# Optimization experiments

Hardware: AMD Instinct MI355X
Metric: run time of the kernel (lower is better)

## Reference

```python
import jax, jax.numpy as jnp
import numpy as np

ENC = 50       # enc_units
TEMP = 5.0     # attention_temp
T = 20         # rollout steps
B = 262144


def setup_inputs() -> dict:
    key = jax.random.key(0)
    ks = jax.random.split(key, 16)
    u = lambda k, shape, lo, hi: jax.random.uniform(k, shape, minval=lo, maxval=hi, dtype=jnp.float32)
    n = lambda k, shape, s: jax.random.normal(k, shape, dtype=jnp.float32) * s
    return {
        "unscaled_s": u(ks[0], (B, T, 7), 0.1, 2.0),          # vel/dv/dx features, kept positive
        "z": n(ks[1], (B, 2), 1.0),
        "desired_v": u(ks[2], (B, 1), 10.0, 30.0),
        "desired_tgap": u(ks[3], (B, 1), 0.5, 2.0),
        "min_jamx": u(ks[4], (B, 1), 1.0, 4.0),
        "max_act": u(ks[5], (B, 1), 0.5, 3.0),
        "min_act": u(ks[6], (B, 1), 0.5, 3.0),
        "h0": n(ks[7], (B, ENC), 0.1),
        "c0": n(ks[8], (B, ENC), 0.1),
        "W_lstm": n(ks[9], (2, 4 * ENC), 0.3),
        "U_lstm": n(ks[10], (ENC, 4 * ENC), 0.1),
        "b_lstm": jnp.zeros((4 * ENC,), jnp.float32),
        "W_att": n(ks[11], (ENC, ENC), 0.1),
        "b_att": jnp.zeros((ENC,), jnp.float32),
        "W_neu": n(ks[12], (ENC, 1), 0.1),
        "b_neu": jnp.zeros((1,), jnp.float32),
    }


def reference(unscaled_s, z, desired_v, desired_tgap, min_jamx, max_act, min_act,
              h0, c0, W_lstm, U_lstm, b_lstm, W_att, b_att, W_neu, b_neu):
    def idm(vel, dv, dx):  # all [B,1]
        gap = min_jamx + desired_tgap * vel + vel * dv / (2.0 * jnp.sqrt(max_act * min_act))
        act = max_act * (1.0 - (vel / desired_v) ** 4 - (gap / dx) ** 2)
        return jnp.clip(act, -3.5, 3.5)

    # LSTM input z is the same every step: precompute input contribution once.
    xz = z @ W_lstm + b_lstm  # [B, 4*ENC]

    def step(carry, s_t):  # s_t: [B, 7]
        h, c = carry
        gates = xz + h @ U_lstm
        i, f, g, o = jnp.split(gates, 4, axis=-1)  # keras gate order i,f,c,o
        c = jax.nn.sigmoid(f) * c + jax.nn.sigmoid(i) * jnp.tanh(g)
        h = jax.nn.sigmoid(o) * jnp.tanh(c)
        att = jax.nn.sigmoid(TEMP * ((h @ W_att + b_att) @ W_neu + b_neu))  # [B,1]
        vel = s_t[:, 0:1]
        fl = idm(vel, s_t[:, 2:3], s_t[:, 3:4])
        fm = idm(vel, s_t[:, 5:6], s_t[:, 6:7])
        act = att * fl + (1.0 - att) * fm
        return (h, c), (act, att)

    (_, _), (acts, atts) = jax.lax.scan(step, (h0, c0), jnp.transpose(unscaled_s, (1, 0, 2)))
    act_seq = jnp.transpose(acts, (1, 0, 2))    # [B, T, 1]
    att_scores = jnp.transpose(atts, (1, 0, 2))  # [B, T, 1]
    return act_seq, att_scores
```

## Files before the change

### kernel.cpp

```cpp
#include <hip/hip_runtime.h>

#define ENC 50
#define NT 20
#define TEMPC 5.0f
#define HSTRIDE 72
#define L2E 1.4426950408889634f
#define NFRAG 26

typedef __attribute__((ext_vector_type(8))) short bf16x8;
typedef __attribute__((ext_vector_type(4))) float f32x4;

__device__ __forceinline__ unsigned short f2bf(float x) {
  union { float f; unsigned u; } cv; cv.f = x;
  unsigned u = cv.u;
  u += 0x7FFFu + ((u >> 16) & 1u);
  return (unsigned short)(u >> 16);
}

__global__ void idm_prep(const float* __restrict__ U, const float* __restrict__ Wl,
                         const float* __restrict__ bl, const float* __restrict__ Wa,
                         const float* __restrict__ ba, const float* __restrict__ Wn,
                         const float* __restrict__ bn,
                         unsigned short* __restrict__ Afrag, float* __restrict__ wcomb) {
  int tid = blockIdx.x * blockDim.x + threadIdx.x;
  for (int idx = tid; idx < NFRAG * 64; idx += blockDim.x * gridDim.x) {
    int frag = idx >> 6, lane = idx & 63;
    int m = frag >> 1, kt = frag & 1;
    int sub = lane & 15;
    int kbase = 32 * kt + 8 * (lane >> 4);
    int p = sub >> 2, q = sub & 3;
    int f = 4 * m + p;
    float sc = (q == 2) ? (2.0f * L2E) : (-L2E);
    unsigned short o[8];
#pragma unroll
    for (int e = 0; e < 8; ++e) {
      int k = kbase + e;
      float val = 0.f;
      if (f < ENC) {
        int col = q * ENC + f;
        if (k < ENC)            val = U[k * 4 * ENC + col];
        else if (k == ENC)      val = Wl[col];
        else if (k == ENC + 1)  val = Wl[4 * ENC + col];
        else if (k == ENC + 2)  val = bl[col];
      }
      o[e] = f2bf(val * sc);
    }
#pragma unroll
    for (int e = 0; e < 8; ++e) Afrag[idx * 8 + e] = o[e];
  }
  if (tid < 52) {
    float s = 0.f;
    if (tid < ENC) { for (int j = 0; j < ENC; ++j) s += Wa[tid * ENC + j] * Wn[j]; }
    wcomb[tid] = s * (-TEMPC * L2E);
  }
  if (tid == 52) {
    float s = bn[0];
    for (int j = 0; j < ENC; ++j) s += ba[j] * Wn[j];
    wcomb[52] = s * (-TEMPC * L2E);
  }
}

template <int PRE>
__global__ __launch_bounds__(256, 2) void idm_main(
    const float* __restrict__ s_in, const float* __restrict__ zin,
    const float* __restrict__ dvp, const float* __restrict__ tgp,
    const float* __restrict__ jxp, const float* __restrict__ map,
    const float* __restrict__ mip, const float* __restrict__ h0,
    const float* __restrict__ c0,
    const unsigned short* __restrict__ Afrag, const float* __restrict__ wcomb,
    const float* __restrict__ U, const float* __restrict__ Wl, const float* __restrict__ bl,
    const float* __restrict__ Wa, const float* __restrict__ ba,
    const float* __restrict__ Wn, const float* __restrict__ bn,
    float* __restrict__ out_act, float* __restrict__ out_att, int Btot) {
  __shared__ __align__(16) unsigned short hlds[4 * 16 * HSTRIDE];
  __shared__ float wcl[64];
  const int tid = threadIdx.x;
  const int wid = tid >> 6, lane = tid & 63;
  const int v = lane & 15, p = lane >> 4;
  int b = blockIdx.x * 64 + wid * 16 + v;
  if (b >= Btot) b = Btot - 1;

  bf16x8 A[13][2];
  float wc[13], bcomb;
  if (PRE) {
#pragma unroll
    for (int m = 0; m < 13; ++m) {
      A[m][0] = ((const bf16x8*)Afrag)[(2 * m) * 64 + lane];
      A[m][1] = ((const bf16x8*)Afrag)[(2 * m + 1) * 64 + lane];
    }
#pragma unroll
    for (int m = 0; m < 13; ++m) { int f = 4 * m + p; wc[m] = (f < ENC) ? wcomb[f] : 0.f; }
    bcomb = wcomb[52];
  } else {
    if (tid < 53) {
      float s;
      if (tid < ENC) {
        s = 0.f;
        for (int j = 0; j < ENC; ++j) s += Wa[tid * ENC + j] * Wn[j];
      } else if (tid < 52) {
        s = 0.f;
      } else {
        s = bn[0];
        for (int j = 0; j < ENC; ++j) s += ba[j] * Wn[j];
      }
      wcl[tid] = s * (-TEMPC * L2E);
    } else if (tid < 64) {
      wcl[tid] = 0.f;
    }
    __syncthreads();
#pragma unroll
    for (int m = 0; m < 13; ++m) {
#pragma unroll
      for (int kt = 0; kt < 2; ++kt) {
        const int pp = v >> 2, q = v & 3;
        const int fb = 4 * m + pp;
        const int kbase = 32 * kt + 8 * p;
        float sc = (q == 2) ? (2.0f * L2E) : (-L2E);
        bf16x8 a;
#pragma unroll
        for (int e = 0; e < 8; ++e) {
          int k = kbase + e;
          float val = 0.f;
          if (fb < ENC) {
            int col = q * ENC + fb;
            if (k < ENC)            val = U[k * 4 * ENC + col];
            else if (k == ENC)      val = Wl[col];
            else if (k == ENC + 1)  val = Wl[4 * ENC + col];
            else if (k == ENC + 2)  val = bl[col];
          }
          a[e] = (short)f2bf(val * sc);
        }
        A[m][kt] = a;
      }
    }
#pragma unroll
    for (int m = 0; m < 13; ++m) { int f = 4 * m + p; wc[m] = (f < ENC) ? wcl[f] : 0.f; }
    bcomb = wcl[52];
  }

  const float amax = map[b], amin = mip[b];
  const float tgap = tgp[b], jamx = jxp[b];
  const float inv_dv = __builtin_amdgcn_rcpf(dvp[b]);
  const float inv2s = 0.5f * __builtin_amdgcn_rsqf(amax * amin);

  float c[13];
#pragma unroll
  for (int m = 0; m < 13; ++m) {
    int f = 4 * m + p;
    c[m] = (f < ENC) ? c0[(size_t)b * ENC + f] : 0.f;
  }

  unsigned short* hl = &hlds[wid * 16 * HSTRIDE];
  for (int i = lane; i < 16 * HSTRIDE / 2; i += 64) ((unsigned*)hl)[i] = 0u;
#pragma unroll
  for (int m = 0; m < 13; ++m) {
    int f = 4 * m + p;
    if (f < ENC) hl[v * HSTRIDE + f] = f2bf(h0[(size_t)b * ENC + f]);
  }
  if (p == 0) {
    hl[v * HSTRIDE + 50] = f2bf(zin[(size_t)b * 2 + 0]);
    hl[v * HSTRIDE + 51] = f2bf(zin[(size_t)b * 2 + 1]);
    hl[v * HSTRIDE + 52] = (unsigned short)0x3F80;
  }

  const float* srow = s_in + (size_t)b * (NT * 7);
  const size_t ob = (size_t)b * NT;
  const bf16x8* hv = (const bf16x8*)hl;
  const int sel = 3 * (p & 1);

#pragma unroll 1
  for (int t = 0; t < NT; ++t) {
    bf16x8 B0 = hv[v * 9 + p];
    bf16x8 B1 = hv[v * 9 + 4 + p];
    f32x4 accbuf[2];
    {
      f32x4 z4 = {0.f, 0.f, 0.f, 0.f};
      f32x4 t0 = __builtin_amdgcn_mfma_f32_16x16x32_bf16(A[0][0], B0, z4, 0, 0, 0);
      accbuf[0] = __builtin_amdgcn_mfma_f32_16x16x32_bf16(A[0][1], B1, t0, 0, 0, 0);
    }
    float att_dot = 0.f;
#pragma unroll
    for (int m = 0; m < 13; ++m) {
      if (m < 12) {
        f32x4 z4 = {0.f, 0.f, 0.f, 0.f};
        f32x4 t0 = __builtin_amdgcn_mfma_f32_16x16x32_bf16(A[m + 1][0], B0, z4, 0, 0, 0);
        accbuf[(m + 1) & 1] = __builtin_amdgcn_mfma_f32_16x16x32_bf16(A[m + 1][1], B1, t0, 0, 0, 0);
      }
      f32x4 acc = accbuf[m & 1];
      float a  = __builtin_amdgcn_exp2f(acc[0]);
      float bb = __builtin_amdgcn_exp2f(acc[1]);
      float G  = __builtin_amdgcn_exp2f(acc[2]);
      float d  = __builtin_amdgcn_exp2f(acc[3]);
      float R = 1.f + a, P = 1.f + bb, Q = G + 1.f;
      float QR = Q * R;
      float num = fmaf(G - 1.f, P, c[m] * QR);
      float cn = num * __builtin_amdgcn_rcpf(P * QR);
      c[m] = cn;
      float C2 = __builtin_amdgcn_exp2f(cn * (2.0f * L2E));
      float hn = (C2 - 1.f) * __builtin_amdgcn_rcpf((C2 + 1.f) * (1.f + d));
      att_dot = fmaf(hn, wc[m], att_dot);
      int f = 4 * m + p;
      if (f < ENC) hl[v * HSTRIDE + f] = f2bf(hn);
    }
    att_dot += __shfl_xor(att_dot, 16, 64);
    att_dot += __shfl_xor(att_dot, 32, 64);
    float e2 = __builtin_amdgcn_exp2f(att_dot + bcomb);
    float att = __builtin_amdgcn_rcpf(1.f + e2);

    const float* sp = srow + t * 7;
    float vel = sp[0];
    float dvs = sp[2 + sel], dxs = sp[3 + sel];
    float r = vel * inv_dv;
    float r2 = r * r;
    float r4 = r2 * r2;
    float base = jamx + tgap * vel;
    float g = (base + vel * dvs * inv2s) * __builtin_amdgcn_rcpf(dxs);
    float fs = amax * (1.f - r4 - g * g);
    fs = fminf(fmaxf(fs, -3.5f), 3.5f);
    float fo = __shfl_xor(fs, 16, 64);
    float act = att * fs + (1.f - att) * fo;
    if (p == 0) {
      out_act[ob + t] = act;
      out_att[ob + t] = att;
    }
  }
}

extern "C" void kernel_launch(void* const* d_in, const int* in_sizes, int n_in,
                              void* d_out, int out_size, void* d_ws, size_t ws_size,
                              hipStream_t stream) {
  const float* s   = (const float*)d_in[0];
  const float* z   = (const float*)d_in[1];
  const float* dv  = (const float*)d_in[2];
  const float* tg  = (const float*)d_in[3];
  const float* jx  = (const float*)d_in[4];
  const float* ma  = (const float*)d_in[5];
  const float* mi  = (const float*)d_in[6];
  const float* h0  = (const float*)d_in[7];
  const float* c0  = (const float*)d_in[8];
  const float* Wl  = (const float*)d_in[9];
  const float* Ul  = (const float*)d_in[10];
  const float* bl  = (const float*)d_in[11];
  const float* Wa  = (const float*)d_in[12];
  const float* ba  = (const float*)d_in[13];
  const float* Wn  = (const float*)d_in[14];
  const float* bn  = (const float*)d_in[15];
  const int B = in_sizes[2];
  float* out_act = (float*)d_out;
  float* out_att = out_act + (size_t)B * NT;
  const int grid = (B + 63) / 64;
  const size_t need = (size_t)NFRAG * 64 * 8 * sizeof(unsigned short) + 64 * sizeof(float);
  if (d_ws && ws_size >= need) {
    unsigned short* Af = (unsigned short*)d_ws;
    float* wcb = (float*)(Af + NFRAG * 64 * 8);
    idm_prep<<<1, 256, 0, stream>>>(Ul, Wl, bl, Wa, ba, Wn, bn, Af, wcb);
    idm_main<1><<<grid, 256, 0, stream>>>(s, z, dv, tg, jx, ma, mi, h0, c0, Af, wcb,
                                          Ul, Wl, bl, Wa, ba, Wn, bn, out_act, out_att, B);
  } else {
    idm_main<0><<<grid, 256, 0, stream>>>(s, z, dv, tg, jx, ma, mi, h0, c0, nullptr, nullptr,
                                          Ul, Wl, bl, Wa, ba, Wn, bn, out_act, out_att, B);
  }
}
```

Measured before the change: 353.7 us.

## Move half of LSTM weight fragments to LDS and remap features for packed stores

Only 6 of the 13 weight-tile fragment pairs stay in registers; the other 7 are staged into shared memory once per block and read every step. This frees VGPRs so launch bounds can rise from 2 to 3 blocks per SM for more latency hiding. The hidden-feature layout is remapped to contiguous 13-feature chunks per lane group so pairs of h values can be stored as one packed bf16 word. In exchange, each step issues extra LDS reads on the serial recurrence path.

```diff
diff --git a/kernel.cpp b/kernel.cpp
--- a/kernel.cpp
+++ b/kernel.cpp
@@ -5,7 +5,9 @@
 #define TEMPC 5.0f
 #define HSTRIDE 72
 #define L2E 1.4426950408889634f
-#define NFRAG 26
+#define NTILE 13
+#define NREG 6
+#define NLDS 7
 
 typedef __attribute__((ext_vector_type(8))) short bf16x8;
 typedef __attribute__((ext_vector_type(4))) float f32x4;
@@ -15,6 +17,27 @@
   unsigned u = cv.u;
   u += 0x7FFFu + ((u >> 16) & 1u);
   return (unsigned short)(u >> 16);
+}
+
+__device__ __forceinline__ float a_elem(int m, int lane, int kt, int e,
+                                        const float* U, const float* Wl,
+                                        const float* bl) {
+  int sub = lane & 15;
+  int pa = sub >> 2, r = sub & 3;
+  int feat = 13 * pa + m;
+  int k = 32 * kt + 8 * (lane >> 4) + e;
+  float val = 0.f;
+  if (feat < ENC) {
+    int col = r * ENC + feat;
+    if (k < 56) {
+      int pk = k / 14, j = k - 14 * pk;
+      int fin = 13 * pk + j;
+      if (j < 13 && fin < ENC) val = U[fin * 4 * ENC + col];
+    } else if (k == 56) val = Wl[col];
+    else if (k == 57)   val = Wl[4 * ENC + col];
+    else if (k == 58)   val = bl[col];
+  }
+  return val * ((r == 2) ? (2.0f * L2E) : (-L2E));
 }
 
 __global__ void idm_prep(const float* __restrict__ U, const float* __restrict__ Wl,
@@ -23,28 +46,12 @@
                          const float* __restrict__ bn,
                          unsigned short* __restrict__ Afrag, float* __restrict__ wcomb) {
   int tid = blockIdx.x * blockDim.x + threadIdx.x;
-  for (int idx = tid; idx < NFRAG * 64; idx += blockDim.x * gridDim.x) {
+  for (int idx = tid; idx < 2 * NTILE * 64; idx += blockDim.x * gridDim.x) {
     int frag = idx >> 6, lane = idx & 63;
     int m = frag >> 1, kt = frag & 1;
-    int sub = lane & 15;
-    int kbase = 32 * kt + 8 * (lane >> 4);
-    int p = sub >> 2, q = sub & 3;
-    int f = 4 * m + p;
-    float sc = (q == 2) ? (2.0f * L2E) : (-L2E);
     unsigned short o[8];
 #pragma unroll
-    for (int e = 0; e < 8; ++e) {
-      int k = kbase + e;
-      float val = 0.f;
-      if (f < ENC) {
-        int col = q * ENC + f;
-        if (k < ENC)            val = U[k * 4 * ENC + col];
-        else if (k == ENC)      val = Wl[col];
-        else if (k == ENC + 1)  val = Wl[4 * ENC + col];
-        else if (k == ENC + 2)  val = bl[col];
-      }
-      o[e] = f2bf(val * sc);
-    }
+    for (int e = 0; e < 8; ++e) o[e] = f2bf(a_elem(m, lane, kt, e, U, Wl, bl));
 #pragma unroll
     for (int e = 0; e < 8; ++e) Afrag[idx * 8 + e] = o[e];
   }
@@ -61,7 +68,7 @@
 }
 
 template <int PRE>
-__global__ __launch_bounds__(256, 2) void idm_main(
+__global__ __launch_bounds__(256, 3) void idm_main(
     const float* __restrict__ s_in, const float* __restrict__ zin,
     const float* __restrict__ dvp, const float* __restrict__ tgp,
     const float* __restrict__ jxp, const float* __restrict__ map,
@@ -72,6 +79,7 @@
     const float* __restrict__ Wa, const float* __restrict__ ba,
     const float* __restrict__ Wn, const float* __restrict__ bn,
     float* __restrict__ out_act, float* __restrict__ out_att, int Btot) {
+  __shared__ __align__(16) unsigned short AldT[NLDS * 2 * 64 * 8];
   __shared__ __align__(16) unsigned short hlds[4 * 16 * HSTRIDE];
   __shared__ float wcl[64];
   const int tid = threadIdx.x;
@@ -80,16 +88,21 @@
   int b = blockIdx.x * 64 + wid * 16 + v;
   if (b >= Btot) b = Btot - 1;
 
-  bf16x8 A[13][2];
-  float wc[13], bcomb;
+  bf16x8 Ar[NREG][2];
+  float wc[NTILE], bcomb;
   if (PRE) {
 #pragma unroll
-    for (int m = 0; m < 13; ++m) {
-      A[m][0] = ((const bf16x8*)Afrag)[(2 * m) * 64 + lane];
-      A[m][1] = ((const bf16x8*)Afrag)[(2 * m + 1) * 64 + lane];
-    }
-#pragma unroll
-    for (int m = 0; m < 13; ++m) { int f = 4 * m + p; wc[m] = (f < ENC) ? wcomb[f] : 0.f; }
+    for (int m = 0; m < NREG; ++m) {
+      Ar[m][0] = ((const bf16x8*)Afrag)[(2 * m) * 64 + lane];
+      Ar[m][1] = ((const bf16x8*)Afrag)[(2 * m + 1) * 64 + lane];
+    }
+    {
+      f32x4* dst = (f32x4*)AldT;
+      const f32x4* src = (const f32x4*)Afrag + NREG * 2 * 64;
+      for (int i = tid; i < NLDS * 2 * 64; i += 256) dst[i] = src[i];
+    }
+#pragma unroll
+    for (int m = 0; m < NTILE; ++m) wc[m] = wcomb[13 * p + m];
     bcomb = wcomb[52];
   } else {
     if (tid < 53) {
@@ -107,84 +120,92 @@
     } else if (tid < 64) {
       wcl[tid] = 0.f;
     }
+#pragma unroll
+    for (int m = 0; m < NREG; ++m) {
+#pragma unroll
+      for (int kt = 0; kt < 2; ++kt) {
+        bf16x8 a;
+#pragma unroll
+        for (int e = 0; e < 8; ++e) a[e] = (short)f2bf(a_elem(m, lane, kt, e, U, Wl, bl));
+        Ar[m][kt] = a;
+      }
+    }
+    for (int q = wid; q < NLDS * 2; q += 4) {
+      int m = NREG + (q >> 1), kt = q & 1;
+      unsigned short o[8];
+#pragma unroll
+      for (int e = 0; e < 8; ++e) o[e] = f2bf(a_elem(m, lane, kt, e, U, Wl, bl));
+      bf16x8 a;
+#pragma unroll
+      for (int e = 0; e < 8; ++e) a[e] = (short)o[e];
+      ((bf16x8*)AldT)[q * 64 + lane] = a;
+    }
     __syncthreads();
 #pragma unroll
-    for (int m = 0; m < 13; ++m) {
-#pragma unroll
-      for (int kt = 0; kt < 2; ++kt) {
-        const int pp = v >> 2, q = v & 3;
-        const int fb = 4 * m + pp;
-        const int kbase = 32 * kt + 8 * p;
-        float sc = (q == 2) ? (2.0f * L2E) : (-L2E);
-        bf16x8 a;
-#pragma unroll
-        for (int e = 0; e < 8; ++e) {
-          int k = kbase + e;
-          float val = 0.f;
-          if (fb < ENC) {
-            int col = q * ENC + fb;
-            if (k < ENC)            val = U[k * 4 * ENC + col];
-            else if (k == ENC)      val = Wl[col];
-            else if (k == ENC + 1)  val = Wl[4 * ENC + col];
-            else if (k == ENC + 2)  val = bl[col];
-          }
-          a[e] = (short)f2bf(val * sc);
-        }
-        A[m][kt] = a;
-      }
-    }
-#pragma unroll
-    for (int m = 0; m < 13; ++m) { int f = 4 * m + p; wc[m] = (f < ENC) ? wcl[f] : 0.f; }
+    for (int m = 0; m < NTILE; ++m) wc[m] = wcl[13 * p + m];
     bcomb = wcl[52];
   }
+  __syncthreads();
 
   const float amax = map[b], amin = mip[b];
   const float tgap = tgp[b], jamx = jxp[b];
   const float inv_dv = __builtin_amdgcn_rcpf(dvp[b]);
   const float inv2s = 0.5f * __builtin_amdgcn_rsqf(amax * amin);
 
-  float c[13];
-#pragma unroll
-  for (int m = 0; m < 13; ++m) {
-    int f = 4 * m + p;
+  float c[NTILE];
+#pragma unroll
+  for (int m = 0; m < NTILE; ++m) {
+    int f = 13 * p + m;
     c[m] = (f < ENC) ? c0[(size_t)b * ENC + f] : 0.f;
   }
 
   unsigned short* hl = &hlds[wid * 16 * HSTRIDE];
   for (int i = lane; i < 16 * HSTRIDE / 2; i += 64) ((unsigned*)hl)[i] = 0u;
 #pragma unroll
-  for (int m = 0; m < 13; ++m) {
-    int f = 4 * m + p;
-    if (f < ENC) hl[v * HSTRIDE + f] = f2bf(h0[(size_t)b * ENC + f]);
+  for (int m = 0; m < NTILE; ++m) {
+    int f = 13 * p + m;
+    float h00 = (f < ENC) ? h0[(size_t)b * ENC + f] : 0.f;
+    hl[v * HSTRIDE + 14 * p + m] = f2bf(h00);
   }
   if (p == 0) {
-    hl[v * HSTRIDE + 50] = f2bf(zin[(size_t)b * 2 + 0]);
-    hl[v * HSTRIDE + 51] = f2bf(zin[(size_t)b * 2 + 1]);
-    hl[v * HSTRIDE + 52] = (unsigned short)0x3F80;
+    hl[v * HSTRIDE + 56] = f2bf(zin[(size_t)b * 2 + 0]);
+    hl[v * HSTRIDE + 57] = f2bf(zin[(size_t)b * 2 + 1]);
+    hl[v * HSTRIDE + 58] = (unsigned short)0x3F80;
   }
 
   const float* srow = s_in + (size_t)b * (NT * 7);
   const size_t ob = (size_t)b * NT;
   const bf16x8* hv = (const bf16x8*)hl;
   const int sel = 3 * (p & 1);
+  unsigned* hlw = (unsigned*)hl;
+  const int wbase = v * 36 + 7 * p;
+  unsigned aoff = 0;
 
 #pragma unroll 1
   for (int t = 0; t < NT; ++t) {
+    asm volatile("" : "+v"(aoff));
+    const bf16x8* ATv = (const bf16x8*)AldT + aoff;
     bf16x8 B0 = hv[v * 9 + p];
     bf16x8 B1 = hv[v * 9 + 4 + p];
     f32x4 accbuf[2];
     {
       f32x4 z4 = {0.f, 0.f, 0.f, 0.f};
-      f32x4 t0 = __builtin_amdgcn_mfma_f32_16x16x32_bf16(A[0][0], B0, z4, 0, 0, 0);
-      accbuf[0] = __builtin_amdgcn_mfma_f32_16x16x32_bf16(A[0][1], B1, t0, 0, 0, 0);
+      f32x4 t0 = __builtin_amdgcn_mfma_f32_16x16x32_bf16(Ar[0][0], B0, z4, 0, 0, 0);
+      accbuf[0] = __builtin_amdgcn_mfma_f32_16x16x32_bf16(Ar[0][1], B1, t0, 0, 0, 0);
     }
     float att_dot = 0.f;
-#pragma unroll
-    for (int m = 0; m < 13; ++m) {
-      if (m < 12) {
-        f32x4 z4 = {0.f, 0.f, 0.f, 0.f};
-        f32x4 t0 = __builtin_amdgcn_mfma_f32_16x16x32_bf16(A[m + 1][0], B0, z4, 0, 0, 0);
-        accbuf[(m + 1) & 1] = __builtin_amdgcn_mfma_f32_16x16x32_bf16(A[m + 1][1], B1, t0, 0, 0, 0);
+    float hprev = 0.f;
+#pragma unroll
+    for (int m = 0; m < NTILE; ++m) {
+      bf16x8 x0, x1;
+      if (m < NTILE - 1) {
+        if (m + 1 < NREG) {
+          x0 = Ar[m + 1][0]; x1 = Ar[m + 1][1];
+        } else {
+          int q = (m + 1 - NREG) * 2;
+          x0 = ATv[q * 64 + lane];
+          x1 = ATv[(q + 1) * 64 + lane];
+        }
       }
       f32x4 acc = accbuf[m & 1];
       float a  = __builtin_amdgcn_exp2f(acc[0]);
@@ -199,8 +220,20 @@
       float C2 = __builtin_amdgcn_exp2f(cn * (2.0f * L2E));
       float hn = (C2 - 1.f) * __builtin_amdgcn_rcpf((C2 + 1.f) * (1.f + d));
       att_dot = fmaf(hn, wc[m], att_dot);
-      int f = 4 * m + p;
-      if (f < ENC) hl[v * HSTRIDE + f] = f2bf(hn);
+      if (m & 1) {
+        unsigned pk;
+        asm("v_cvt_pk_bf16_f32 %0, %1, %2" : "=v"(pk) : "v"(hprev), "v"(hn));
+        hlw[wbase + (m >> 1)] = pk;
+      } else if (m == NTILE - 1) {
+        hl[v * HSTRIDE + 14 * p + 12] = f2bf(hn);
+      } else {
+        hprev = hn;
+      }
+      if (m < NTILE - 1) {
+        f32x4 z4 = {0.f, 0.f, 0.f, 0.f};
+        f32x4 t0 = __builtin_amdgcn_mfma_f32_16x16x32_bf16(x0, B0, z4, 0, 0, 0);
+        accbuf[(m + 1) & 1] = __builtin_amdgcn_mfma_f32_16x16x32_bf16(x1, B1, t0, 0, 0, 0);
+      }
     }
     att_dot += __shfl_xor(att_dot, 16, 64);
     att_dot += __shfl_xor(att_dot, 32, 64);
@@ -249,10 +282,10 @@
   float* out_act = (float*)d_out;
   float* out_att = out_act + (size_t)B * NT;
   const int grid = (B + 63) / 64;
-  const size_t need = (size_t)NFRAG * 64 * 8 * sizeof(unsigned short) + 64 * sizeof(float);
+  const size_t need = (size_t)2 * NTILE * 64 * 8 * sizeof(unsigned short) + 64 * sizeof(float);
   if (d_ws && ws_size >= need) {
     unsigned short* Af = (unsigned short*)d_ws;
-    float* wcb = (float*)(Af + NFRAG * 64 * 8);
+    float* wcb = (float*)(Af + 2 * NTILE * 64 * 8);
     idm_prep<<<1, 256, 0, stream>>>(Ul, Wl, bl, Wa, ba, Wn, bn, Af, wcb);
     idm_main<1><<<grid, 256, 0, stream>>>(s, z, dv, tg, jx, ma, mi, h0, c0, Af, wcb,
                                           Ul, Wl, bl, Wa, ba, Wn, bn, out_act, out_att, B);
```

Result: faster. 300.5 us (-15.0%).
